# Optimization experiments

Hardware: AMD Instinct MI355X
Metric: run time of the kernel (lower is better)

Reference implementation:

```python
import jax, jax.numpy as jnp
import numpy as np

B, S, E, H = 4, 1024, 768, 8
HD = E // H
FF = 4 * E
SCALING = HD ** -0.5


def _layernorm(x, g, b, eps=1e-5):
    m = jnp.mean(x, axis=-1, keepdims=True)
    v = jnp.var(x, axis=-1, keepdims=True)
    return (x - m) / jnp.sqrt(v + eps) * g + b


def setup_inputs() -> dict:
    key = jax.random.key(0)
    ks = jax.random.split(key, 12)
    w = lambda k, shp: (jax.random.normal(k, shp, jnp.float32) * 0.02)
    return {
        "x": jax.random.normal(ks[0], (B, S, E), jnp.float32),
        "dist_map": jax.random.uniform(ks[1], (B, H, S, S), jnp.float32),
        "mask": jnp.zeros((B, S), jnp.int32),
        "Wq": w(ks[2], (E, E)), "bq": jnp.zeros((E,), jnp.float32),
        "Wk": w(ks[3], (E, E)), "bk": jnp.zeros((E,), jnp.float32),
        "Wv": w(ks[4], (E, E)), "bv": jnp.zeros((E,), jnp.float32),
        "Wo": w(ks[5], (E, E)), "bo": jnp.zeros((E,), jnp.float32),
        "ln1_g": jnp.ones((E,), jnp.float32), "ln1_b": jnp.zeros((E,), jnp.float32),
        "W1": w(ks[6], (FF, E)), "b1": jnp.zeros((FF,), jnp.float32),
        "W2": w(ks[7], (E, FF)), "b2": jnp.zeros((E,), jnp.float32),
        "ln2_g": jnp.ones((E,), jnp.float32), "ln2_b": jnp.zeros((E,), jnp.float32),
    }


def reference(x, dist_map, mask, Wq, bq, Wk, bk, Wv, bv, Wo, bo,
              ln1_g, ln1_b, W1, b1, W2, b2, ln2_g, ln2_b):
    # --- attention residual block (pre-norm) ---
    h = _layernorm(x, ln1_g, ln1_b)
    # NOTE: torch does .view(B, H, S, HD) directly on [B, S, E] -> pure reshape, no transpose
    q = (h @ Wq.T + bq).reshape(B, H, S, HD)
    k = (h @ Wk.T + bk).reshape(B, H, S, HD)
    v = (h @ Wv.T + bv).reshape(B, H, S, HD)
    attn_weights = jnp.einsum("bhqd,bhkd->bhqk", q, k)
    pad = mask.astype(bool)[:, None, None, :]          # [B,1,1,S]
    attn_weights = jnp.where(pad, -10000.0, attn_weights)  # mask BEFORE scaling (as in source)
    probs = jax.nn.softmax(attn_weights * SCALING, axis=-1)
    probs = (probs + dist_map) * 0.5                   # post-softmax dist bias
    ctx = jnp.einsum("bhal,bhlv->bhav", probs, v)      # [B,H,S,HD]
    ctx = ctx.transpose(0, 2, 1, 3).reshape(B, S, E)
    x1 = x + (ctx @ Wo.T + bo)
    # --- FFN residual block (pre-norm) ---
    h2 = _layernorm(x1, ln2_g, ln2_b)
    ffn = jax.nn.gelu(h2 @ W1.T + b1, approximate=False) @ W2.T + b2
    out = x1 + ffn
    return out, probs
```

## Files before the change

### kernel.cpp

```cpp
#include <hip/hip_runtime.h>
#include <math.h>

typedef unsigned short u16;
typedef u16   u16x8  __attribute__((ext_vector_type(8)));
typedef u16   u16x4  __attribute__((ext_vector_type(4)));
typedef __bf16 bf16x8 __attribute__((ext_vector_type(8)));
typedef float f32x4  __attribute__((ext_vector_type(4)));

#define SZ_BSE   3145728
#define HEADSZ   98304
#define SCALING  0.10206207261596577f

__device__ __forceinline__ u16 f2bf(float f) {
  union { float f; unsigned u; } c; c.f = f;
  unsigned u = c.u;
  return (u16)((u + 0x7fffu + ((u >> 16) & 1u)) >> 16);
}
__device__ __forceinline__ float bf2f(u16 v) {
  union { unsigned u; float f; } c; c.u = ((unsigned)v) << 16; return c.f;
}

typedef const __attribute__((address_space(1))) unsigned int* gas1_t;
typedef __attribute__((address_space(3))) unsigned int* las3_t;
__device__ __forceinline__ void gload16(const void* g, void* l) {
  __builtin_amdgcn_global_load_lds((gas1_t)g, (las3_t)l, 16, 0, 0);
}

__global__ __launch_bounds__(256) void cvt_k(const float* __restrict__ in,
                                             u16* __restrict__ out, int n) {
  int i = (blockIdx.x * 256 + threadIdx.x) * 4;
  if (i >= n) return;
  f32x4 v = *(const f32x4*)&in[i];
  u16x4 o; o[0]=f2bf(v[0]); o[1]=f2bf(v[1]); o[2]=f2bf(v[2]); o[3]=f2bf(v[3]);
  *(u16x4*)&out[i] = o;
}

__global__ __launch_bounds__(256) void ln_k(const float* __restrict__ x,
                                            const float* __restrict__ g,
                                            const float* __restrict__ b,
                                            u16* __restrict__ out) {
  const int row = blockIdx.x;
  const float* xr = x + (long)row * 768;
  const int t = threadIdx.x;
  float v0 = xr[t], v1 = xr[t + 256], v2 = xr[t + 512];
  float s = v0 + v1 + v2, ss = v0*v0 + v1*v1 + v2*v2;
  for (int o = 32; o > 0; o >>= 1) { s += __shfl_xor(s, o); ss += __shfl_xor(ss, o); }
  __shared__ float red[8];
  int w = t >> 6;
  if ((t & 63) == 0) { red[w] = s; red[w + 4] = ss; }
  __syncthreads();
  s  = red[0] + red[1] + red[2] + red[3];
  ss = red[4] + red[5] + red[6] + red[7];
  float mean = s * (1.0f / 768.0f);
  float var  = ss * (1.0f / 768.0f) - mean * mean;
  float rstd = rsqrtf(var + 1e-5f);
  u16* orow = out + (long)row * 768;
  orow[t]       = f2bf((v0 - mean) * rstd * g[t]       + b[t]);
  orow[t + 256] = f2bf((v1 - mean) * rstd * g[t + 256] + b[t + 256]);
  orow[t + 512] = f2bf((v2 - mean) * rstd * g[t + 512] + b[t + 512]);
}

__global__ __launch_bounds__(256) void vtrans_k(const u16* __restrict__ v,
                                                u16* __restrict__ vt) {
  __shared__ u16 tile[64 * 98];
  const int z = blockIdx.x >> 4;
  const int s0 = (blockIdx.x & 15) << 6;
  const int t = threadIdx.x;
  const u16* src = v + (long)z * HEADSZ + (long)s0 * 96;
#pragma unroll
  for (int it = 0; it < 3; ++it) {
    int i = it * 2048 + t * 8;
    int s = i / 96, d = i % 96;
    *(u16x8*)&tile[s * 98 + d] = *(const u16x8*)&src[i];
  }
  __syncthreads();
  u16* dst = vt + (long)z * HEADSZ + s0;
#pragma unroll
  for (int it = 0; it < 6; ++it) {
    int o = it * 1024 + t * 4;
    int d = o >> 6, s = o & 63;
    u16x4 wv;
#pragma unroll
    for (int j = 0; j < 4; ++j) wv[j] = tile[(s + j) * 98 + d];
    *(u16x4*)&dst[(long)d * 1024 + s] = wv;
  }
}

__global__ __launch_bounds__(256) void reduce_k(const float* __restrict__ p,
                                                const float* __restrict__ resid,
                                                const float* __restrict__ bias,
                                                float* __restrict__ out) {
  long i = ((long)blockIdx.x * 256 + threadIdx.x) * 4;
  f32x4 a = *(const f32x4*)&p[i];
  f32x4 b = *(const f32x4*)&p[3145728 + i];
  f32x4 c = *(const f32x4*)&p[6291456 + i];
  f32x4 r = *(const f32x4*)&resid[i];
  int cb = (int)(i % 768);
  f32x4 g = *(const f32x4*)&bias[cb];
  f32x4 o;
  o[0] = r[0] + g[0] + a[0] + b[0] + c[0];
  o[1] = r[1] + g[1] + a[1] + b[1] + c[1];
  o[2] = r[2] + g[2] + a[2] + b[2] + c[2];
  o[3] = r[3] + g[3] + a[3] + b[3] + c[3];
  *(f32x4*)&out[i] = o;
}

__global__ __launch_bounds__(512, 4)
void attn_k(const u16* __restrict__ qb, const u16* __restrict__ kb,
            const u16* __restrict__ vT, const float* __restrict__ dist,
            const int* __restrict__ maskp, float* __restrict__ probs,
            u16* __restrict__ ctx) {
  __shared__ u16 sP[8 * 16 * 72];
  __shared__ float sX[4 * 64 * 24];
  __shared__ float sSum[2][64];
  __shared__ u16 sFlag[1024];

  const int t = threadIdx.x;
  const int z = blockIdx.y;
  const int r0 = blockIdx.x * 64;
  const int b = z >> 3, h = z & 7;

  {
    const int* mp = maskp + b * 1024 + t * 2;
    int2 mv = *(const int2*)mp;
    sFlag[t * 2]     = (u16)(mv.x != 0);
    sFlag[t * 2 + 1] = (u16)(mv.y != 0);
  }
  __syncthreads();

  const int lane = t & 63;
  const int w = t >> 6;
  const int rs = w & 3, ch = w >> 2;
  const int wr0 = rs * 16;
  const int lr = lane & 15;
  const int lg = lane >> 4;
  const int cbase = ch * 512;
  u16* sPw = sP + w * (16 * 72);

  const u16* qh = qb + (long)z * HEADSZ;
  const u16* kh = kb + (long)z * HEADSZ;
  const u16* vh = vT + (long)z * HEADSZ;
  const float* dh = dist + (long)z * 1048576;
  float* ph = probs + (long)z * 1048576;

  bf16x8 qa[3];
  {
    const u16* qr = qh + (long)(r0 + wr0 + lr) * 96 + lg * 8;
#pragma unroll
    for (int kf = 0; kf < 3; ++kf) qa[kf] = *(const bf16x8*)(qr + kf * 32);
  }

  const float neg = -10000.0f * SCALING;
  float srun[4] = {0.f, 0.f, 0.f, 0.f};

  for (int c = 0; c < 8; ++c) {
    const int c0 = cbase + c * 64;
    f32x4 a4[4] = {};
#pragma unroll
    for (int ni = 0; ni < 4; ++ni) {
      const u16* kr = kh + (long)(c0 + ni * 16 + lr) * 96 + lg * 8;
#pragma unroll
      for (int kf = 0; kf < 3; ++kf)
        a4[ni] = __builtin_amdgcn_mfma_f32_16x16x32_bf16(
            qa[kf], *(const bf16x8*)(kr + kf * 32), a4[ni], 0, 0, 0);
    }
#pragma unroll
    for (int ni = 0; ni < 4; ++ni) {
      bool fm = sFlag[c0 + ni * 16 + lr] != 0;
#pragma unroll
      for (int r = 0; r < 4; ++r) {
        float sv = fm ? neg : a4[ni][r] * SCALING;
        srun[r] += __expf(sv);
      }
    }
  }
#pragma unroll
  for (int r = 0; r < 4; ++r) {
    float s = srun[r];
    s += __shfl_xor(s, 1);
    s += __shfl_xor(s, 2);
    s += __shfl_xor(s, 4);
    s += __shfl_xor(s, 8);
    if (lr == 0) sSum[ch][wr0 + lg * 4 + r] = s;
  }
  __syncthreads();
  float inv[4];
#pragma unroll
  for (int r = 0; r < 4; ++r)
    inv[r] = 1.0f / (sSum[0][wr0 + lg * 4 + r] + sSum[1][wr0 + lg * 4 + r]);

  const int lrow = lane >> 2;
  const int cg   = (lane & 3) * 16;
  f32x4 cacc[6] = {};
  for (int c = 0; c < 8; ++c) {
    const int c0 = cbase + c * 64;
    f32x4 a4[4] = {};
#pragma unroll
    for (int ni = 0; ni < 4; ++ni) {
      const u16* kr = kh + (long)(c0 + ni * 16 + lr) * 96 + lg * 8;
#pragma unroll
      for (int kf = 0; kf < 3; ++kf)
        a4[ni] = __builtin_amdgcn_mfma_f32_16x16x32_bf16(
            qa[kf], *(const bf16x8*)(kr + kf * 32), a4[ni], 0, 0, 0);
    }
#pragma unroll
    for (int ni = 0; ni < 4; ++ni) {
      bool fm = sFlag[c0 + ni * 16 + lr] != 0;
#pragma unroll
      for (int r = 0; r < 4; ++r) {
        float sv = fm ? neg : a4[ni][r] * SCALING;
        sPw[(lg * 4 + r) * 72 + ni * 16 + lr] = f2bf(__expf(sv) * inv[r]);
      }
    }
    {
      u16x8 e0 = *(const u16x8*)&sPw[lrow * 72 + cg];
      u16x8 e1 = *(const u16x8*)&sPw[lrow * 72 + cg + 8];
      const float* dp = dh + (long)(r0 + wr0 + lrow) * 1024 + c0 + cg;
      float* pp = ph + (long)(r0 + wr0 + lrow) * 1024 + c0 + cg;
      f32x4 d0 = *(const f32x4*)dp;
      f32x4 d1 = *(const f32x4*)(dp + 4);
      f32x4 d2 = *(const f32x4*)(dp + 8);
      f32x4 d3 = *(const f32x4*)(dp + 12);
      f32x4 p0, p1, p2, p3;
#pragma unroll
      for (int j = 0; j < 4; ++j) {
        p0[j] = (bf2f(e0[j])     + d0[j]) * 0.5f;
        p1[j] = (bf2f(e0[4 + j]) + d1[j]) * 0.5f;
        p2[j] = (bf2f(e1[j])     + d2[j]) * 0.5f;
        p3[j] = (bf2f(e1[4 + j]) + d3[j]) * 0.5f;
      }
      *(f32x4*)pp        = p0;
      *(f32x4*)(pp + 4)  = p1;
      *(f32x4*)(pp + 8)  = p2;
      *(f32x4*)(pp + 12) = p3;
      u16x8 o0, o1;
#pragma unroll
      for (int j = 0; j < 4; ++j) {
        o0[j]     = f2bf(p0[j]);
        o0[4 + j] = f2bf(p1[j]);
        o1[j]     = f2bf(p2[j]);
        o1[4 + j] = f2bf(p3[j]);
      }
      *(u16x8*)&sPw[lrow * 72 + cg]     = o0;
      *(u16x8*)&sPw[lrow * 72 + cg + 8] = o1;
    }
#pragma unroll
    for (int ks = 0; ks < 2; ++ks) {
      bf16x8 pa = *(const bf16x8*)&sPw[lr * 72 + ks * 32 + lg * 8];
      const u16* vr = vh + (long)lr * 1024 + c0 + ks * 32 + lg * 8;
#pragma unroll
      for (int n2 = 0; n2 < 6; ++n2) {
        bf16x8 vb = *(const bf16x8*)(vr + (long)n2 * 16 * 1024);
        cacc[n2] = __builtin_amdgcn_mfma_f32_16x16x32_bf16(pa, vb, cacc[n2], 0, 0, 0);
      }
    }
  }

  __syncthreads();
  if (ch == 1) {
    float* xp = sX + ((rs * 64 + lane) * 24);
#pragma unroll
    for (int n2 = 0; n2 < 6; ++n2) *(f32x4*)&xp[n2 * 4] = cacc[n2];
  }
  __syncthreads();
  if (ch == 0) {
    const float* xp = sX + ((rs * 64 + lane) * 24);
    u16* cbp = ctx + (long)b * 786432 + h * 96;
#pragma unroll
    for (int n2 = 0; n2 < 6; ++n2) {
      f32x4 xv = *(const f32x4*)&xp[n2 * 4];
      int d = n2 * 16 + lr;
#pragma unroll
      for (int r = 0; r < 4; ++r)
        cbp[(long)(r0 + wr0 + lg * 4 + r) * 768 + d] = f2bf(cacc[n2][r] + xv[r]);
    }
  }
}

enum { EPI_QKV = 0, EPI_GELU = 1, EPI_PARTIAL = 2 };

template <int EPI>
__global__ __launch_bounds__(256, 2)
void gemm_k(const u16* __restrict__ A, int lda,
            const u16* __restrict__ W, int ldw,
            void* __restrict__ Cv, long sCz, int ldc,
            const float* __restrict__ bias,
            int N, int K, int kchunks) {
  __shared__ u16 sA[4096];
  __shared__ u16 sB[4096];

  const int t  = threadIdx.x;
  const int kc = blockIdx.z;
  const int klen = K / kchunks;
  const int kbeg = kc * klen, kend = kbeg + klen;
  const int m0 = blockIdx.x * 128;
  const int n0 = blockIdx.y * 128;

  const int r0 = t >> 2;
  const int c0 = (t & 3) << 3;
  char* lA = (char*)sA + ((t >> 6) << 10);
  char* lB = (char*)sB + ((t >> 6) << 10);

  int bn0 = n0 + r0;      if (bn0 > N - 1) bn0 = N - 1;
  int bn1 = n0 + 64 + r0; if (bn1 > N - 1) bn1 = N - 1;
  const u16* gB0 = W + (long)bn0 * ldw + c0;
  const u16* gB1 = W + (long)bn1 * ldw + c0;
  const u16* gA0 = A + (long)(m0 + r0) * lda + c0;
  const u16* gA1 = gA0 + 64 * lda;

  const int lane = t & 63;
  const int w  = t >> 6;
  const int wm = (w >> 1) * 64, wn = (w & 1) * 64;
  const int lr = lane & 15, lg = lane >> 4;

  f32x4 acc[4][4] = {};

  for (int k0 = kbeg; k0 < kend; k0 += 32) {
    gload16(gA0 + k0, lA);
    gload16(gA1 + k0, lA + 4096);
    gload16(gB0 + k0, lB);
    gload16(gB1 + k0, lB + 4096);
    __syncthreads();

    bf16x8 aF[4], bF[4];
#pragma unroll
    for (int mi = 0; mi < 4; ++mi)
      aF[mi] = *(const bf16x8*)&sA[(wm + mi * 16 + lr) * 32 + lg * 8];
#pragma unroll
    for (int ni = 0; ni < 4; ++ni)
      bF[ni] = *(const bf16x8*)&sB[(wn + ni * 16 + lr) * 32 + lg * 8];
#pragma unroll
    for (int mi = 0; mi < 4; ++mi)
#pragma unroll
      for (int ni = 0; ni < 4; ++ni)
        acc[mi][ni] = __builtin_amdgcn_mfma_f32_16x16x32_bf16(aF[mi], bF[ni], acc[mi][ni], 0, 0, 0);
    __syncthreads();
  }

  long coff = (EPI == EPI_PARTIAL) ? (long)kc * sCz : 0;

#pragma unroll
  for (int mi = 0; mi < 4; ++mi) {
#pragma unroll
    for (int ni = 0; ni < 4; ++ni) {
      int gc = n0 + wn + ni * 16 + lr;
      if (gc >= N) continue;
      int gr0 = m0 + wm + mi * 16 + lg * 4;
#pragma unroll
      for (int r = 0; r < 4; ++r) {
        float vv = acc[mi][ni][r];
        if (EPI == EPI_QKV) {
          vv += bias[gc];
          int wsel = gc >= 1536 ? 2 : (gc >= 768 ? 1 : 0);
          int c = gc - wsel * 768;
          ((u16*)Cv)[(long)wsel * 3145728 + (long)(gr0 + r) * 768 + c] = f2bf(vv);
        } else if (EPI == EPI_GELU) {
          vv += bias[gc];
          vv = 0.5f * vv * (1.0f + erff(vv * 0.70710678118654752f));
          ((u16*)Cv)[coff + (long)(gr0 + r) * ldc + gc] = f2bf(vv);
        } else {
          ((float*)Cv)[coff + (long)(gr0 + r) * ldc + gc] = vv;
        }
      }
    }
  }
}

extern "C" void kernel_launch(void* const* d_in, const int* in_sizes, int n_in,
                              void* d_out, int out_size, void* d_ws, size_t ws_size,
                              hipStream_t stream) {
  (void)in_sizes; (void)n_in; (void)out_size; (void)ws_size;
  const float* x    = (const float*)d_in[0];
  const float* dist = (const float*)d_in[1];
  const int*   mask = (const int*)d_in[2];
  const float* Wq = (const float*)d_in[3];  const float* bq  = (const float*)d_in[4];
  const float* Wk = (const float*)d_in[5];  const float* bk  = (const float*)d_in[6];
  const float* Wv = (const float*)d_in[7];  const float* bv  = (const float*)d_in[8];
  const float* Wo = (const float*)d_in[9];  const float* bo  = (const float*)d_in[10];
  const float* g1 = (const float*)d_in[11]; const float* b1n = (const float*)d_in[12];
  const float* W1 = (const float*)d_in[13]; const float* b1f = (const float*)d_in[14];
  const float* W2 = (const float*)d_in[15]; const float* b2f = (const float*)d_in[16];
  const float* g2 = (const float*)d_in[17]; const float* b2n = (const float*)d_in[18];

  char* ws = (char*)d_ws;
  u16*   h    = (u16*)(ws + 0);
  u16*   ctx  = (u16*)(ws + 0);
  u16*   qkv  = (u16*)(ws + 6291456);
  u16*   q    = qkv;
  u16*   k    = (u16*)(ws + 12582912);
  u16*   v    = (u16*)(ws + 18874368);
  u16*   vT   = (u16*)(ws + 25165824);
  float* part = (float*)(ws + 6291456);
  u16*   h2   = (u16*)(ws + 31457280);
  u16*   ffn1 = (u16*)(ws + 44040192);
  float* x1   = (float*)(ws + 69206016);
  u16*   wqkvb= (u16*)(ws + 81788928);
  u16*   wob  = (u16*)(ws + 85327872);
  u16*   w1b  = (u16*)(ws + 86507520);
  u16*   w2b  = (u16*)(ws + 91226112);
  float* bqkv = (float*)(ws + 95944704);

  float* outp   = (float*)d_out;
  float* probs  = outp + SZ_BSE;

  cvt_k<<<576,  256, 0, stream>>>(Wq, wqkvb,           589824);
  cvt_k<<<576,  256, 0, stream>>>(Wk, wqkvb + 589824,  589824);
  cvt_k<<<576,  256, 0, stream>>>(Wv, wqkvb + 1179648, 589824);
  cvt_k<<<576,  256, 0, stream>>>(Wo, wob, 589824);
  cvt_k<<<2304, 256, 0, stream>>>(W1, w1b, 2359296);
  cvt_k<<<2304, 256, 0, stream>>>(W2, w2b, 2359296);
  hipMemcpyAsync(bqkv,        bq, 3072, hipMemcpyDeviceToDevice, stream);
  hipMemcpyAsync(bqkv + 768,  bk, 3072, hipMemcpyDeviceToDevice, stream);
  hipMemcpyAsync(bqkv + 1536, bv, 3072, hipMemcpyDeviceToDevice, stream);

  ln_k<<<4096, 256, 0, stream>>>(x, g1, b1n, h);

  gemm_k<EPI_QKV><<<dim3(32, 18, 1), 256, 0, stream>>>(
      h, 768, wqkvb, 768, qkv, 0, 768, bqkv, 2304, 768, 1);

  vtrans_k<<<512, 256, 0, stream>>>(v, vT);

  attn_k<<<dim3(16, 32), 512, 0, stream>>>(q, k, vT, dist, mask, probs, ctx);

  gemm_k<EPI_PARTIAL><<<dim3(32, 6, 3), 256, 0, stream>>>(
      ctx, 768, wob, 768, part, 3145728, 768, nullptr, 768, 768, 3);
  reduce_k<<<3072, 256, 0, stream>>>(part, x, bo, x1);

  ln_k<<<4096, 256, 0, stream>>>(x1, g2, b2n, h2);

  gemm_k<EPI_GELU><<<dim3(32, 24, 1), 256, 0, stream>>>(
      h2, 768, w1b, 768, ffn1, 0, 3072, b1f, 3072, 768, 1);

  gemm_k<EPI_PARTIAL><<<dim3(32, 6, 3), 256, 0, stream>>>(
      ffn1, 3072, w2b, 3072, part, 3145728, 768, nullptr, 768, 3072, 3);
  reduce_k<<<3072, 256, 0, stream>>>(part, x1, b2f, outp);
}
```

Measured before the change: 332.5 us.

## Split attention into scores, probs and PV kernels to avoid recomputing QK^T

Replaces the fused two-pass attention kernel with three kernels: one computes QK^T once and stashes unnormalized bf16 exponentials in the upper half of the probs output rows along with per-row inverse sums, one normalizes and adds the distance bias in place, and one reads the fp32 probs back to multiply by V. This removes the second QK^T recomputation. In exchange it adds substantial extra global memory traffic and two kernel launches.

```diff
diff --git a/kernel.cpp b/kernel.cpp
--- a/kernel.cpp
+++ b/kernel.cpp
@@ -106,19 +106,17 @@
 }
 
 __global__ __launch_bounds__(512, 4)
-void attn_k(const u16* __restrict__ qb, const u16* __restrict__ kb,
-            const u16* __restrict__ vT, const float* __restrict__ dist,
-            const int* __restrict__ maskp, float* __restrict__ probs,
-            u16* __restrict__ ctx) {
+void scores_k(const u16* __restrict__ qb, const u16* __restrict__ kb,
+              const int* __restrict__ maskp, float* __restrict__ probs,
+              float* __restrict__ rowsInv) {
   __shared__ u16 sP[8 * 16 * 72];
-  __shared__ float sX[4 * 64 * 24];
   __shared__ float sSum[2][64];
   __shared__ u16 sFlag[1024];
 
   const int t = threadIdx.x;
   const int z = blockIdx.y;
   const int r0 = blockIdx.x * 64;
-  const int b = z >> 3, h = z & 7;
+  const int b = z >> 3;
 
   {
     const int* mp = maskp + b * 1024 + t * 2;
@@ -132,16 +130,15 @@
   const int w = t >> 6;
   const int rs = w & 3, ch = w >> 2;
   const int wr0 = rs * 16;
-  const int lr = lane & 15;
-  const int lg = lane >> 4;
+  const int lr = lane & 15, lg = lane >> 4;
   const int cbase = ch * 512;
   u16* sPw = sP + w * (16 * 72);
+  const int lrow = lane >> 2;
+  const int cg = (lane & 3) * 16;
 
   const u16* qh = qb + (long)z * HEADSZ;
   const u16* kh = kb + (long)z * HEADSZ;
-  const u16* vh = vT + (long)z * HEADSZ;
-  const float* dh = dist + (long)z * 1048576;
-  float* ph = probs + (long)z * 1048576;
+  u16* eb = (u16*)probs + (long)z * 2097152;
 
   bf16x8 qa[3];
   {
@@ -170,10 +167,18 @@
 #pragma unroll
       for (int r = 0; r < 4; ++r) {
         float sv = fm ? neg : a4[ni][r] * SCALING;
-        srun[r] += __expf(sv);
+        float e = __expf(sv);
+        srun[r] += e;
+        sPw[(lg * 4 + r) * 72 + ni * 16 + lr] = f2bf(e);
       }
     }
-  }
+    u16x8 e0 = *(const u16x8*)&sPw[lrow * 72 + cg];
+    u16x8 e1 = *(const u16x8*)&sPw[lrow * 72 + cg + 8];
+    u16* ep = eb + (long)(r0 + wr0 + lrow) * 2048 + 1024 + c0 + cg;
+    *(u16x8*)ep       = e0;
+    *(u16x8*)(ep + 8) = e1;
+  }
+
 #pragma unroll
   for (int r = 0; r < 4; ++r) {
     float s = srun[r];
@@ -184,86 +189,88 @@
     if (lr == 0) sSum[ch][wr0 + lg * 4 + r] = s;
   }
   __syncthreads();
-  float inv[4];
-#pragma unroll
-  for (int r = 0; r < 4; ++r)
-    inv[r] = 1.0f / (sSum[0][wr0 + lg * 4 + r] + sSum[1][wr0 + lg * 4 + r]);
-
-  const int lrow = lane >> 2;
-  const int cg   = (lane & 3) * 16;
+  if (ch == 0 && lr == 0) {
+#pragma unroll
+    for (int r = 0; r < 4; ++r) {
+      float iv = 1.0f / (sSum[0][wr0 + lg * 4 + r] + sSum[1][wr0 + lg * 4 + r]);
+      rowsInv[(long)z * 1024 + r0 + wr0 + lg * 4 + r] = iv;
+    }
+  }
+}
+
+__global__ __launch_bounds__(256)
+void probs_k(float* __restrict__ probs, const float* __restrict__ dist,
+             const float* __restrict__ rowsInv) {
+  const long row = blockIdx.x;
+  float* pr = probs + row * 1024;
+  const float* dr = dist + row * 1024;
+  const float iv = rowsInv[row];
+  const int t = threadIdx.x;
+  u16x4 ev = *(const u16x4*)((const u16*)pr + 1024 + t * 4);
+  f32x4 dv = *(const f32x4*)&dr[t * 4];
+  asm volatile("s_waitcnt vmcnt(0)" ::: "memory");
+  __syncthreads();
+  f32x4 o;
+#pragma unroll
+  for (int j = 0; j < 4; ++j) o[j] = (bf2f(ev[j]) * iv + dv[j]) * 0.5f;
+  *(f32x4*)&pr[t * 4] = o;
+}
+
+__global__ __launch_bounds__(512, 4)
+void pv_k(const float* __restrict__ probs, const u16* __restrict__ vT,
+          u16* __restrict__ ctx) {
+  __shared__ float sX[4 * 64 * 24];
+  const int t = threadIdx.x;
+  const int z = blockIdx.y;
+  const int r0 = blockIdx.x * 64;
+  const int b = z >> 3, h = z & 7;
+  const int lane = t & 63, w = t >> 6;
+  const int rs = w & 3, kh = w >> 2;
+  const int wr0 = rs * 16;
+  const int lr = lane & 15, lg = lane >> 4;
+
+  const float* ph = probs + (long)z * 1048576 + (long)(r0 + wr0 + lr) * 1024 + lg * 8;
+  const u16* vh = vT + (long)z * HEADSZ;
+  const int cb = kh * 512;
+
   f32x4 cacc[6] = {};
+#pragma unroll
   for (int c = 0; c < 8; ++c) {
-    const int c0 = cbase + c * 64;
-    f32x4 a4[4] = {};
-#pragma unroll
-    for (int ni = 0; ni < 4; ++ni) {
-      const u16* kr = kh + (long)(c0 + ni * 16 + lr) * 96 + lg * 8;
-#pragma unroll
-      for (int kf = 0; kf < 3; ++kf)
-        a4[ni] = __builtin_amdgcn_mfma_f32_16x16x32_bf16(
-            qa[kf], *(const bf16x8*)(kr + kf * 32), a4[ni], 0, 0, 0);
-    }
-#pragma unroll
-    for (int ni = 0; ni < 4; ++ni) {
-      bool fm = sFlag[c0 + ni * 16 + lr] != 0;
-#pragma unroll
-      for (int r = 0; r < 4; ++r) {
-        float sv = fm ? neg : a4[ni][r] * SCALING;
-        sPw[(lg * 4 + r) * 72 + ni * 16 + lr] = f2bf(__expf(sv) * inv[r]);
-      }
-    }
-    {
-      u16x8 e0 = *(const u16x8*)&sPw[lrow * 72 + cg];
-      u16x8 e1 = *(const u16x8*)&sPw[lrow * 72 + cg + 8];
-      const float* dp = dh + (long)(r0 + wr0 + lrow) * 1024 + c0 + cg;
-      float* pp = ph + (long)(r0 + wr0 + lrow) * 1024 + c0 + cg;
-      f32x4 d0 = *(const f32x4*)dp;
-      f32x4 d1 = *(const f32x4*)(dp + 4);
-      f32x4 d2 = *(const f32x4*)(dp + 8);
-      f32x4 d3 = *(const f32x4*)(dp + 12);
-      f32x4 p0, p1, p2, p3;
-#pragma unroll
-      for (int j = 0; j < 4; ++j) {
-        p0[j] = (bf2f(e0[j])     + d0[j]) * 0.5f;
-        p1[j] = (bf2f(e0[4 + j]) + d1[j]) * 0.5f;
-        p2[j] = (bf2f(e1[j])     + d2[j]) * 0.5f;
-        p3[j] = (bf2f(e1[4 + j]) + d3[j]) * 0.5f;
-      }
-      *(f32x4*)pp        = p0;
-      *(f32x4*)(pp + 4)  = p1;
-      *(f32x4*)(pp + 8)  = p2;
-      *(f32x4*)(pp + 12) = p3;
-      u16x8 o0, o1;
-#pragma unroll
-      for (int j = 0; j < 4; ++j) {
-        o0[j]     = f2bf(p0[j]);
-        o0[4 + j] = f2bf(p1[j]);
-        o1[j]     = f2bf(p2[j]);
-        o1[4 + j] = f2bf(p3[j]);
-      }
-      *(u16x8*)&sPw[lrow * 72 + cg]     = o0;
-      *(u16x8*)&sPw[lrow * 72 + cg + 8] = o1;
-    }
-#pragma unroll
-    for (int ks = 0; ks < 2; ++ks) {
-      bf16x8 pa = *(const bf16x8*)&sPw[lr * 72 + ks * 32 + lg * 8];
-      const u16* vr = vh + (long)lr * 1024 + c0 + ks * 32 + lg * 8;
-#pragma unroll
-      for (int n2 = 0; n2 < 6; ++n2) {
-        bf16x8 vb = *(const bf16x8*)(vr + (long)n2 * 16 * 1024);
-        cacc[n2] = __builtin_amdgcn_mfma_f32_16x16x32_bf16(pa, vb, cacc[n2], 0, 0, 0);
-      }
-    }
-  }
-
-  __syncthreads();
-  if (ch == 1) {
+    const int c0 = cb + c * 64;
+    const float* pp = ph + c0;
+    f32x4 p0 = *(const f32x4*)pp;
+    f32x4 p1 = *(const f32x4*)(pp + 4);
+    f32x4 p2 = *(const f32x4*)(pp + 32);
+    f32x4 p3 = *(const f32x4*)(pp + 36);
+    u16x8 w0, w1;
+#pragma unroll
+    for (int j = 0; j < 4; ++j) {
+      w0[j] = f2bf(p0[j]); w0[4 + j] = f2bf(p1[j]);
+      w1[j] = f2bf(p2[j]); w1[4 + j] = f2bf(p3[j]);
+    }
+    bf16x8 pa0 = *(bf16x8*)&w0;
+    bf16x8 pa1 = *(bf16x8*)&w1;
+    const u16* vr0 = vh + (long)lr * 1024 + c0 + lg * 8;
+#pragma unroll
+    for (int n2 = 0; n2 < 6; ++n2) {
+      bf16x8 vb = *(const bf16x8*)(vr0 + (long)n2 * 16384);
+      cacc[n2] = __builtin_amdgcn_mfma_f32_16x16x32_bf16(pa0, vb, cacc[n2], 0, 0, 0);
+    }
+#pragma unroll
+    for (int n2 = 0; n2 < 6; ++n2) {
+      bf16x8 vb = *(const bf16x8*)(vr0 + 32 + (long)n2 * 16384);
+      cacc[n2] = __builtin_amdgcn_mfma_f32_16x16x32_bf16(pa1, vb, cacc[n2], 0, 0, 0);
+    }
+  }
+
+  __syncthreads();
+  if (kh == 1) {
     float* xp = sX + ((rs * 64 + lane) * 24);
 #pragma unroll
     for (int n2 = 0; n2 < 6; ++n2) *(f32x4*)&xp[n2 * 4] = cacc[n2];
   }
   __syncthreads();
-  if (ch == 0) {
+  if (kh == 0) {
     const float* xp = sX + ((rs * 64 + lane) * 24);
     u16* cbp = ctx + (long)b * 786432 + h * 96;
 #pragma unroll
@@ -399,6 +406,7 @@
   u16*   w1b  = (u16*)(ws + 86507520);
   u16*   w2b  = (u16*)(ws + 91226112);
   float* bqkv = (float*)(ws + 95944704);
+  float* rowsInv = (float*)(ws + 95953920);
 
   float* outp   = (float*)d_out;
   float* probs  = outp + SZ_BSE;
@@ -420,7 +428,9 @@
 
   vtrans_k<<<512, 256, 0, stream>>>(v, vT);
 
-  attn_k<<<dim3(16, 32), 512, 0, stream>>>(q, k, vT, dist, mask, probs, ctx);
+  scores_k<<<dim3(16, 32), 512, 0, stream>>>(q, k, mask, probs, rowsInv);
+  probs_k<<<32768, 256, 0, stream>>>(probs, dist, rowsInv);
+  pv_k<<<dim3(16, 32), 512, 0, stream>>>(probs, vT, ctx);
 
   gemm_k<EPI_PARTIAL><<<dim3(32, 6, 3), 256, 0, stream>>>(
       ctx, 768, wob, 768, part, 3145728, 768, nullptr, 768, 768, 3);
```

New measurement: 328.3 us. Within noise of the previous version (-1.2%).

## Split attention into scores and PV kernels, fuse V transpose into QKV GEMM

Applied to the files above, without the earlier changes.

The attention kernel no longer recomputes QK^T twice. A scores kernel now writes unnormalized exp values straight into the probs output and stores per-row inverse sums, and a second kernel reads them back, normalizes, adds dist_map and does the PV MFMA. The V transpose kernel is folded into the QKV GEMM epilogue through a scattered store, and the six weight conversions are merged into one launch. This trades the duplicated matmul work for an extra full fp32 probs write-plus-read pass (16 MB each way), and it adds strided, poorly coalesced stores in the GEMM epilogue.

```diff
diff --git a/kernel.cpp b/kernel.cpp
--- a/kernel.cpp
+++ b/kernel.cpp
@@ -26,13 +26,20 @@
   __builtin_amdgcn_global_load_lds((gas1_t)g, (las3_t)l, 16, 0, 0);
 }
 
-__global__ __launch_bounds__(256) void cvt_k(const float* __restrict__ in,
-                                             u16* __restrict__ out, int n) {
-  int i = (blockIdx.x * 256 + threadIdx.x) * 4;
-  if (i >= n) return;
-  f32x4 v = *(const f32x4*)&in[i];
+struct CvtArgs {
+  const float* src[6];
+  u16* dst[6];
+};
+__global__ __launch_bounds__(256) void cvtall_k(CvtArgs a) {
+  int bid = blockIdx.x;
+  int which, base;
+  if (bid < 2304)      { which = bid / 576; base = (bid - which * 576) * 1024; }
+  else if (bid < 4608) { which = 4; base = (bid - 2304) * 1024; }
+  else                 { which = 5; base = (bid - 4608) * 1024; }
+  int i = base + threadIdx.x * 4;
+  f32x4 v = *(const f32x4*)&a.src[which][i];
   u16x4 o; o[0]=f2bf(v[0]); o[1]=f2bf(v[1]); o[2]=f2bf(v[2]); o[3]=f2bf(v[3]);
-  *(u16x4*)&out[i] = o;
+  *(u16x4*)&a.dst[which][i] = o;
 }
 
 __global__ __launch_bounds__(256) void ln_k(const float* __restrict__ x,
@@ -60,32 +67,6 @@
   orow[t + 512] = f2bf((v2 - mean) * rstd * g[t + 512] + b[t + 512]);
 }
 
-__global__ __launch_bounds__(256) void vtrans_k(const u16* __restrict__ v,
-                                                u16* __restrict__ vt) {
-  __shared__ u16 tile[64 * 98];
-  const int z = blockIdx.x >> 4;
-  const int s0 = (blockIdx.x & 15) << 6;
-  const int t = threadIdx.x;
-  const u16* src = v + (long)z * HEADSZ + (long)s0 * 96;
-#pragma unroll
-  for (int it = 0; it < 3; ++it) {
-    int i = it * 2048 + t * 8;
-    int s = i / 96, d = i % 96;
-    *(u16x8*)&tile[s * 98 + d] = *(const u16x8*)&src[i];
-  }
-  __syncthreads();
-  u16* dst = vt + (long)z * HEADSZ + s0;
-#pragma unroll
-  for (int it = 0; it < 6; ++it) {
-    int o = it * 1024 + t * 4;
-    int d = o >> 6, s = o & 63;
-    u16x4 wv;
-#pragma unroll
-    for (int j = 0; j < 4; ++j) wv[j] = tile[(s + j) * 98 + d];
-    *(u16x4*)&dst[(long)d * 1024 + s] = wv;
-  }
-}
-
 __global__ __launch_bounds__(256) void reduce_k(const float* __restrict__ p,
                                                 const float* __restrict__ resid,
                                                 const float* __restrict__ bias,
@@ -106,19 +87,16 @@
 }
 
 __global__ __launch_bounds__(512, 4)
-void attn_k(const u16* __restrict__ qb, const u16* __restrict__ kb,
-            const u16* __restrict__ vT, const float* __restrict__ dist,
-            const int* __restrict__ maskp, float* __restrict__ probs,
-            u16* __restrict__ ctx) {
-  __shared__ u16 sP[8 * 16 * 72];
-  __shared__ float sX[4 * 64 * 24];
+void scores_k(const u16* __restrict__ qb, const u16* __restrict__ kb,
+              const int* __restrict__ maskp, float* __restrict__ probs,
+              float* __restrict__ rowsInv) {
   __shared__ float sSum[2][64];
   __shared__ u16 sFlag[1024];
 
   const int t = threadIdx.x;
   const int z = blockIdx.y;
   const int r0 = blockIdx.x * 64;
-  const int b = z >> 3, h = z & 7;
+  const int b = z >> 3;
 
   {
     const int* mp = maskp + b * 1024 + t * 2;
@@ -132,15 +110,11 @@
   const int w = t >> 6;
   const int rs = w & 3, ch = w >> 2;
   const int wr0 = rs * 16;
-  const int lr = lane & 15;
-  const int lg = lane >> 4;
+  const int lr = lane & 15, lg = lane >> 4;
   const int cbase = ch * 512;
-  u16* sPw = sP + w * (16 * 72);
 
   const u16* qh = qb + (long)z * HEADSZ;
   const u16* kh = kb + (long)z * HEADSZ;
-  const u16* vh = vT + (long)z * HEADSZ;
-  const float* dh = dist + (long)z * 1048576;
   float* ph = probs + (long)z * 1048576;
 
   bf16x8 qa[3];
@@ -167,13 +141,17 @@
 #pragma unroll
     for (int ni = 0; ni < 4; ++ni) {
       bool fm = sFlag[c0 + ni * 16 + lr] != 0;
+      float* pp = ph + (long)(r0 + wr0 + lg * 4) * 1024 + c0 + ni * 16 + lr;
 #pragma unroll
       for (int r = 0; r < 4; ++r) {
         float sv = fm ? neg : a4[ni][r] * SCALING;
-        srun[r] += __expf(sv);
+        float e = __expf(sv);
+        srun[r] += e;
+        pp[r * 1024] = e;
       }
     }
   }
+
 #pragma unroll
   for (int r = 0; r < 4; ++r) {
     float s = srun[r];
@@ -184,73 +162,82 @@
     if (lr == 0) sSum[ch][wr0 + lg * 4 + r] = s;
   }
   __syncthreads();
-  float inv[4];
-#pragma unroll
-  for (int r = 0; r < 4; ++r)
-    inv[r] = 1.0f / (sSum[0][wr0 + lg * 4 + r] + sSum[1][wr0 + lg * 4 + r]);
-
+  if (ch == 0 && lr == 0) {
+#pragma unroll
+    for (int r = 0; r < 4; ++r) {
+      float iv = 1.0f / (sSum[0][wr0 + lg * 4 + r] + sSum[1][wr0 + lg * 4 + r]);
+      rowsInv[(long)z * 1024 + r0 + wr0 + lg * 4 + r] = iv;
+    }
+  }
+}
+
+__global__ __launch_bounds__(512, 2)
+void pv2_k(float* __restrict__ probs, const float* __restrict__ dist,
+           const float* __restrict__ rowsInv, const u16* __restrict__ vT,
+           u16* __restrict__ ctx) {
+  __shared__ u16 sP[8 * 16 * 72];
+  __shared__ float sX[4 * 64 * 24];
+
+  const int t = threadIdx.x;
+  const int z = blockIdx.y;
+  const int r0 = blockIdx.x * 64;
+  const int b = z >> 3, h = z & 7;
+  const int lane = t & 63, w = t >> 6;
+  const int rs = w & 3, ch = w >> 2;
+  const int wr0 = rs * 16;
+  const int lr = lane & 15, lg = lane >> 4;
+  const int cbase = ch * 512;
   const int lrow = lane >> 2;
-  const int cg   = (lane & 3) * 16;
+  const int cg = (lane & 3) * 16;
+  u16* sPw = sP + w * (16 * 72);
+
+  float* ph = probs + (long)z * 1048576;
+  const float* dh = dist + (long)z * 1048576;
+  const u16* vh = vT + (long)z * HEADSZ;
+  const float iv = rowsInv[(long)z * 1024 + r0 + wr0 + lrow];
+
   f32x4 cacc[6] = {};
+#pragma unroll
   for (int c = 0; c < 8; ++c) {
     const int c0 = cbase + c * 64;
-    f32x4 a4[4] = {};
-#pragma unroll
-    for (int ni = 0; ni < 4; ++ni) {
-      const u16* kr = kh + (long)(c0 + ni * 16 + lr) * 96 + lg * 8;
-#pragma unroll
-      for (int kf = 0; kf < 3; ++kf)
-        a4[ni] = __builtin_amdgcn_mfma_f32_16x16x32_bf16(
-            qa[kf], *(const bf16x8*)(kr + kf * 32), a4[ni], 0, 0, 0);
-    }
-#pragma unroll
-    for (int ni = 0; ni < 4; ++ni) {
-      bool fm = sFlag[c0 + ni * 16 + lr] != 0;
-#pragma unroll
-      for (int r = 0; r < 4; ++r) {
-        float sv = fm ? neg : a4[ni][r] * SCALING;
-        sPw[(lg * 4 + r) * 72 + ni * 16 + lr] = f2bf(__expf(sv) * inv[r]);
-      }
-    }
-    {
-      u16x8 e0 = *(const u16x8*)&sPw[lrow * 72 + cg];
-      u16x8 e1 = *(const u16x8*)&sPw[lrow * 72 + cg + 8];
-      const float* dp = dh + (long)(r0 + wr0 + lrow) * 1024 + c0 + cg;
-      float* pp = ph + (long)(r0 + wr0 + lrow) * 1024 + c0 + cg;
-      f32x4 d0 = *(const f32x4*)dp;
-      f32x4 d1 = *(const f32x4*)(dp + 4);
-      f32x4 d2 = *(const f32x4*)(dp + 8);
-      f32x4 d3 = *(const f32x4*)(dp + 12);
-      f32x4 p0, p1, p2, p3;
-#pragma unroll
-      for (int j = 0; j < 4; ++j) {
-        p0[j] = (bf2f(e0[j])     + d0[j]) * 0.5f;
-        p1[j] = (bf2f(e0[4 + j]) + d1[j]) * 0.5f;
-        p2[j] = (bf2f(e1[j])     + d2[j]) * 0.5f;
-        p3[j] = (bf2f(e1[4 + j]) + d3[j]) * 0.5f;
-      }
-      *(f32x4*)pp        = p0;
-      *(f32x4*)(pp + 4)  = p1;
-      *(f32x4*)(pp + 8)  = p2;
-      *(f32x4*)(pp + 12) = p3;
-      u16x8 o0, o1;
-#pragma unroll
-      for (int j = 0; j < 4; ++j) {
-        o0[j]     = f2bf(p0[j]);
-        o0[4 + j] = f2bf(p1[j]);
-        o1[j]     = f2bf(p2[j]);
-        o1[4 + j] = f2bf(p3[j]);
-      }
-      *(u16x8*)&sPw[lrow * 72 + cg]     = o0;
-      *(u16x8*)&sPw[lrow * 72 + cg + 8] = o1;
-    }
+    float* pp = ph + (long)(r0 + wr0 + lrow) * 1024 + c0 + cg;
+    const float* dp = dh + (long)(r0 + wr0 + lrow) * 1024 + c0 + cg;
+    f32x4 e0 = *(const f32x4*)pp;
+    f32x4 e1 = *(const f32x4*)(pp + 4);
+    f32x4 e2 = *(const f32x4*)(pp + 8);
+    f32x4 e3 = *(const f32x4*)(pp + 12);
+    f32x4 d0 = *(const f32x4*)dp;
+    f32x4 d1 = *(const f32x4*)(dp + 4);
+    f32x4 d2 = *(const f32x4*)(dp + 8);
+    f32x4 d3 = *(const f32x4*)(dp + 12);
+    f32x4 p0, p1, p2, p3;
+#pragma unroll
+    for (int j = 0; j < 4; ++j) {
+      p0[j] = (e0[j] * iv + d0[j]) * 0.5f;
+      p1[j] = (e1[j] * iv + d1[j]) * 0.5f;
+      p2[j] = (e2[j] * iv + d2[j]) * 0.5f;
+      p3[j] = (e3[j] * iv + d3[j]) * 0.5f;
+    }
+    *(f32x4*)pp        = p0;
+    *(f32x4*)(pp + 4)  = p1;
+    *(f32x4*)(pp + 8)  = p2;
+    *(f32x4*)(pp + 12) = p3;
+    u16x8 o0, o1;
+#pragma unroll
+    for (int j = 0; j < 4; ++j) {
+      o0[j] = f2bf(p0[j]); o0[4 + j] = f2bf(p1[j]);
+      o1[j] = f2bf(p2[j]); o1[4 + j] = f2bf(p3[j]);
+    }
+    *(u16x8*)&sPw[lrow * 72 + cg]     = o0;
+    *(u16x8*)&sPw[lrow * 72 + cg + 8] = o1;
+
 #pragma unroll
     for (int ks = 0; ks < 2; ++ks) {
       bf16x8 pa = *(const bf16x8*)&sPw[lr * 72 + ks * 32 + lg * 8];
       const u16* vr = vh + (long)lr * 1024 + c0 + ks * 32 + lg * 8;
 #pragma unroll
       for (int n2 = 0; n2 < 6; ++n2) {
-        bf16x8 vb = *(const bf16x8*)(vr + (long)n2 * 16 * 1024);
+        bf16x8 vb = *(const bf16x8*)(vr + (long)n2 * 16384);
         cacc[n2] = __builtin_amdgcn_mfma_f32_16x16x32_bf16(pa, vb, cacc[n2], 0, 0, 0);
       }
     }
@@ -285,6 +272,7 @@
             const u16* __restrict__ W, int ldw,
             void* __restrict__ Cv, long sCz, int ldc,
             const float* __restrict__ bias,
+            u16* __restrict__ vt,
             int N, int K, int kchunks) {
   __shared__ u16 sA[4096];
   __shared__ u16 sB[4096];
@@ -351,9 +339,19 @@
         float vv = acc[mi][ni][r];
         if (EPI == EPI_QKV) {
           vv += bias[gc];
-          int wsel = gc >= 1536 ? 2 : (gc >= 768 ? 1 : 0);
-          int c = gc - wsel * 768;
-          ((u16*)Cv)[(long)wsel * 3145728 + (long)(gr0 + r) * 768 + c] = f2bf(vv);
+          if (gc >= 1536) {
+            int c = gc - 1536;
+            int row = gr0 + r, bb = row >> 10, sr = row & 1023;
+            int hh = sr >> 7;
+            int cd = c / 96;
+            int ss = ((sr & 127) << 3) + cd;
+            int dd = c - cd * 96;
+            vt[(long)(bb * 8 + hh) * HEADSZ + (long)dd * 1024 + ss] = f2bf(vv);
+          } else {
+            int wsel = gc >= 768 ? 1 : 0;
+            int c = gc - wsel * 768;
+            ((u16*)Cv)[(long)wsel * 3145728 + (long)(gr0 + r) * 768 + c] = f2bf(vv);
+          }
         } else if (EPI == EPI_GELU) {
           vv += bias[gc];
           vv = 0.5f * vv * (1.0f + erff(vv * 0.70710678118654752f));
@@ -385,10 +383,9 @@
   char* ws = (char*)d_ws;
   u16*   h    = (u16*)(ws + 0);
   u16*   ctx  = (u16*)(ws + 0);
-  u16*   qkv  = (u16*)(ws + 6291456);
-  u16*   q    = qkv;
+  u16*   qk   = (u16*)(ws + 6291456);
+  u16*   q    = qk;
   u16*   k    = (u16*)(ws + 12582912);
-  u16*   v    = (u16*)(ws + 18874368);
   u16*   vT   = (u16*)(ws + 25165824);
   float* part = (float*)(ws + 6291456);
   u16*   h2   = (u16*)(ws + 31457280);
@@ -399,16 +396,17 @@
   u16*   w1b  = (u16*)(ws + 86507520);
   u16*   w2b  = (u16*)(ws + 91226112);
   float* bqkv = (float*)(ws + 95944704);
+  float* rowsInv = (float*)(ws + 95953920);
 
   float* outp   = (float*)d_out;
   float* probs  = outp + SZ_BSE;
 
-  cvt_k<<<576,  256, 0, stream>>>(Wq, wqkvb,           589824);
-  cvt_k<<<576,  256, 0, stream>>>(Wk, wqkvb + 589824,  589824);
-  cvt_k<<<576,  256, 0, stream>>>(Wv, wqkvb + 1179648, 589824);
-  cvt_k<<<576,  256, 0, stream>>>(Wo, wob, 589824);
-  cvt_k<<<2304, 256, 0, stream>>>(W1, w1b, 2359296);
-  cvt_k<<<2304, 256, 0, stream>>>(W2, w2b, 2359296);
+  CvtArgs ca;
+  ca.src[0] = Wq; ca.src[1] = Wk; ca.src[2] = Wv;
+  ca.src[3] = Wo; ca.src[4] = W1; ca.src[5] = W2;
+  ca.dst[0] = wqkvb; ca.dst[1] = wqkvb + 589824; ca.dst[2] = wqkvb + 1179648;
+  ca.dst[3] = wob;   ca.dst[4] = w1b;            ca.dst[5] = w2b;
+  cvtall_k<<<6912, 256, 0, stream>>>(ca);
   hipMemcpyAsync(bqkv,        bq, 3072, hipMemcpyDeviceToDevice, stream);
   hipMemcpyAsync(bqkv + 768,  bk, 3072, hipMemcpyDeviceToDevice, stream);
   hipMemcpyAsync(bqkv + 1536, bv, 3072, hipMemcpyDeviceToDevice, stream);
@@ -416,22 +414,21 @@
   ln_k<<<4096, 256, 0, stream>>>(x, g1, b1n, h);
 
   gemm_k<EPI_QKV><<<dim3(32, 18, 1), 256, 0, stream>>>(
-      h, 768, wqkvb, 768, qkv, 0, 768, bqkv, 2304, 768, 1);
-
-  vtrans_k<<<512, 256, 0, stream>>>(v, vT);
-
-  attn_k<<<dim3(16, 32), 512, 0, stream>>>(q, k, vT, dist, mask, probs, ctx);
+      h, 768, wqkvb, 768, qk, 0, 768, bqkv, vT, 2304, 768, 1);
+
+  scores_k<<<dim3(16, 32), 512, 0, stream>>>(q, k, mask, probs, rowsInv);
+  pv2_k<<<dim3(16, 32), 512, 0, stream>>>(probs, dist, rowsInv, vT, ctx);
 
   gemm_k<EPI_PARTIAL><<<dim3(32, 6, 3), 256, 0, stream>>>(
-      ctx, 768, wob, 768, part, 3145728, 768, nullptr, 768, 768, 3);
+      ctx, 768, wob, 768, part, 3145728, 768, nullptr, nullptr, 768, 768, 3);
   reduce_k<<<3072, 256, 0, stream>>>(part, x, bo, x1);
 
   ln_k<<<4096, 256, 0, stream>>>(x1, g2, b2n, h2);
 
   gemm_k<EPI_GELU><<<dim3(32, 24, 1), 256, 0, stream>>>(
-      h2, 768, w1b, 768, ffn1, 0, 3072, b1f, 3072, 768, 1);
+      h2, 768, w1b, 768, ffn1, 0, 3072, b1f, nullptr, 3072, 768, 1);
 
   gemm_k<EPI_PARTIAL><<<dim3(32, 6, 3), 256, 0, stream>>>(
-      ffn1, 3072, w2b, 3072, part, 3145728, 768, nullptr, 768, 3072, 3);
+      ffn1, 3072, w2b, 3072, part, 3145728, 768, nullptr, nullptr, 768, 3072, 3);
   reduce_k<<<3072, 256, 0, stream>>>(part, x1, b2f, outp);
 }
```

Measured after the change: 341.7 us. 2.8% more time.
